# Kernel optimization log

Hardware: AMD Instinct MI355X
Metric: run time of the kernel (lower is better)

## Reference

```python
import jax, jax.numpy as jnp
import numpy as np

N = 100000      # num_nodes
E = 400000      # num edges
HID = 128       # hidden_channels (== in_channels, memory dim)
OUT = 64        # out_channels (per head)
HEADS = 4
HD = HEADS * OUT  # 256, TransformerConv concat output dim


def _lin(k, fan_in, fan_out):
    return jax.random.normal(k, (fan_in, fan_out), jnp.float32) * 0.02


def setup_inputs() -> dict:
    key = jax.random.key(0)
    ks = jax.random.split(key, 16)
    return {
        "edge_index": jax.random.randint(ks[0], (2, E), 0, N, dtype=jnp.int64),
        "edge_time": jax.random.randint(ks[1], (E, 1), 0, 1000000, dtype=jnp.int64),
        "x": jax.random.normal(ks[2], (N, HID), jnp.float32),
        "memory": jax.random.normal(ks[3], (N, HID), jnp.float32),  # TGN memory table (detached in fwd)
        # TransformerConv params (lin_query / lin_key / lin_value / lin_skip, all with bias)
        "Wq": _lin(ks[4], HID, HD), "bq": jnp.zeros((HD,), jnp.float32),
        "Wk": _lin(ks[5], HID, HD), "bk": jnp.zeros((HD,), jnp.float32),
        "Wv": _lin(ks[6], HID, HD), "bv": jnp.zeros((HD,), jnp.float32),
        "Wskip": _lin(ks[7], HID, HD), "bskip": jnp.zeros((HD,), jnp.float32),
        # rating MLP: Linear(512,128) -> ReLU -> Linear(128,64) -> ReLU -> Linear(64,1)
        "W1": _lin(ks[8], 2 * HD, 128), "b1": jnp.zeros((128,), jnp.float32),
        "W2": _lin(ks[9], 128, 64), "b2": jnp.zeros((64,), jnp.float32),
        "W3": _lin(ks[10], 64, 1), "b3": jnp.zeros((1,), jnp.float32),
    }


def reference(edge_index, edge_time, x, memory,
              Wq, bq, Wk, bk, Wv, bv, Wskip, bskip,
              W1, b1, W2, b2, W3, b3):
    src, dst = edge_index[0], edge_index[1]
    n = x.shape[0]

    # x = memory.detach() + x
    h = memory + x  # [N, HID]

    # TransformerConv (heads=4, concat=True, root_weight=True)
    q = (h @ Wq + bq).reshape(n, HEADS, OUT)
    k = (h @ Wk + bk).reshape(n, HEADS, OUT)
    v = (h @ Wv + bv).reshape(n, HEADS, OUT)

    # per-edge attention scores: messages flow src -> dst, softmax over in-edges of dst
    scores = jnp.sum(q[dst] * k[src], axis=-1) / jnp.sqrt(jnp.float32(OUT))  # [E, H]
    smax = jax.ops.segment_max(scores, dst, num_segments=n)                   # [N, H]
    e = jnp.exp(scores - smax[dst])
    denom = jax.ops.segment_sum(e, dst, num_segments=n)
    alpha = e / (denom[dst] + 1e-16)                                          # [E, H]

    agg = jax.ops.segment_sum(alpha[:, :, None] * v[src], dst, num_segments=n)  # [N, H, OUT]
    out = agg.reshape(n, HD) + (h @ Wskip + bskip)                              # skip connection

    # interaction embeddings + MLP head (dropout inactive at eval)
    inter = jnp.concatenate([out[src], out[dst]], axis=-1)  # [E, 512]
    hdd = jax.nn.relu(inter @ W1 + b1)
    hdd = jax.nn.relu(hdd @ W2 + b2)
    rating = jax.nn.sigmoid(hdd @ W3 + b3) * 4.0 + 1.0
    return rating[:, 0]
```

## Files before the change

kernel.cpp:

```cpp
#include <hip/hip_runtime.h>
#include <math.h>

#define N_NODES 100000
#define N_EDGES 400000
#define HID 128
#define HEADS 4
#define OUT_C 64
#define HD 256
#define SCAN_CHUNK 1024
#define NB_SCAN ((N_NODES + SCAN_CHUNK - 1) / SCAN_CHUNK)

typedef __attribute__((ext_vector_type(8))) short bf16x8;
typedef __attribute__((ext_vector_type(4))) float f32x4;

__device__ __forceinline__ unsigned short fbf(float f) {
    unsigned u = __float_as_uint(f);
    unsigned r = (u + 0x7fffu + ((u >> 16) & 1u)) >> 16;
    return (unsigned short)r;
}
__device__ __forceinline__ float bf2f(unsigned short u) {
    return __uint_as_float(((unsigned)u) << 16);
}

__device__ __forceinline__ void gl_lds16(const void* g, void* l) {
    __builtin_amdgcn_global_load_lds(
        (const __attribute__((address_space(1))) unsigned int*)g,
        (__attribute__((address_space(3))) unsigned int*)l,
        16, 0, 0);
}

__global__ __launch_bounds__(256) void init_zero(int* __restrict__ deg,
                                                 int* __restrict__ cursor) {
    int i = blockIdx.x * 256 + threadIdx.x;
    if (i < N_NODES) { deg[i] = 0; cursor[i] = 0; }
}

__global__ __launch_bounds__(256) void k_deg(const int* __restrict__ ei,
                                             int* __restrict__ deg) {
    int e = blockIdx.x * 256 + threadIdx.x;
    if (e < N_EDGES) atomicAdd(&deg[ei[N_EDGES + e]], 1);
}

__global__ __launch_bounds__(256) void k_scan1(const int* __restrict__ deg,
                                               int* __restrict__ rp,
                                               int* __restrict__ bsum) {
    __shared__ int ts[256];
    int b = blockIdx.x, t = threadIdx.x;
    int base = b * SCAN_CHUNK + t * 4;
    int vv[4];
    int s = 0;
#pragma unroll
    for (int i = 0; i < 4; ++i) {
        int d = (base + i < N_NODES) ? deg[base + i] : 0;
        vv[i] = s;
        s += d;
    }
    ts[t] = s;
    __syncthreads();
    for (int off = 1; off < 256; off <<= 1) {
        int x = (t >= off) ? ts[t - off] : 0;
        __syncthreads();
        ts[t] += x;
        __syncthreads();
    }
    int ex = ts[t] - s;
#pragma unroll
    for (int i = 0; i < 4; ++i)
        if (base + i < N_NODES) rp[base + i] = ex + vv[i];
    if (t == 255) bsum[b] = ts[255];
}

__global__ __launch_bounds__(256) void k_scan2(int* __restrict__ bsum) {
    __shared__ int ts[256];
    int t = threadIdx.x;
    int v = (t < NB_SCAN) ? bsum[t] : 0;
    ts[t] = v;
    __syncthreads();
    for (int off = 1; off < 256; off <<= 1) {
        int x = (t >= off) ? ts[t - off] : 0;
        __syncthreads();
        ts[t] += x;
        __syncthreads();
    }
    if (t < NB_SCAN) bsum[t] = ts[t] - v;
}

__global__ __launch_bounds__(256) void k_scan3(int* __restrict__ rp,
                                               const int* __restrict__ bsum) {
    int i = blockIdx.x * 256 + threadIdx.x;
    if (i < N_NODES) rp[i] += bsum[i / SCAN_CHUNK];
}

__global__ __launch_bounds__(256) void k_bucket(const int* __restrict__ ei,
                                                const int* __restrict__ rp,
                                                int* __restrict__ cursor,
                                                int* __restrict__ csr_src,
                                                int* __restrict__ csr_dst,
                                                int* __restrict__ csr_eid) {
    int e = blockIdx.x * 256 + threadIdx.x;
    if (e >= N_EDGES) return;
    int src = ei[e];
    int d   = ei[N_EDGES + e];
    int idx = atomicAdd(&cursor[d], 1);
    int s   = rp[d] + idx;
    csr_src[s] = src;
    csr_dst[s] = d;
    csr_eid[s] = e;
}

__global__ __launch_bounds__(256) void pack_wg(
    const float* __restrict__ Wq, const float* __restrict__ Wk,
    const float* __restrict__ Wv, const float* __restrict__ Ws,
    unsigned short* __restrict__ Wp) {
    int i = blockIdx.x * 256 + threadIdx.x;
    if (i >= 16384) return;
    int lane = i & 63, nt = (i >> 6) & 15, kt = (i >> 10) & 3, z = i >> 12;
    const float* W = (z == 0) ? Wq : (z == 1) ? Wk : (z == 2) ? Wv : Ws;
    int q = lane >> 4, c = lane & 15;
#pragma unroll
    for (int j = 0; j < 8; ++j)
        Wp[i * 8 + j] = fbf(W[(kt * 32 + q * 8 + j) * HD + nt * 16 + c]);
}

__global__ __launch_bounds__(256) void pack_wc(const float* __restrict__ W1,
                                               unsigned short* __restrict__ Wcp) {
    int i = blockIdx.x * 256 + threadIdx.x;
    if (i >= 8192) return;
    int lane = i & 63, nt = (i >> 6) & 15, kt = i >> 10;
    int q = lane >> 4, c = lane & 15;
    int n = nt * 16 + c;
#pragma unroll
    for (int j = 0; j < 8; ++j) {
        int k = kt * 32 + q * 8 + j;
        float v = (n < 128) ? W1[k * 128 + n] : W1[(k + 256) * 128 + (n - 128)];
        Wcp[i * 8 + j] = fbf(v);
    }
}

__global__ __launch_bounds__(256) void pack_w2(const float* __restrict__ W2,
                                               unsigned short* __restrict__ W2p) {
    int i = blockIdx.x * 256 + threadIdx.x;
    if (i >= 1024) return;
    int lane = i & 63, nt = (i >> 6) & 3, kt = i >> 8;
    int q = lane >> 4, c = lane & 15;
#pragma unroll
    for (int j = 0; j < 8; ++j)
        W2p[i * 8 + j] = fbf(W2[(kt * 32 + q * 8 + j) * 64 + nt * 16 + c]);
}

__global__ __launch_bounds__(256) void k_pre(const float* __restrict__ x,
                                             const float* __restrict__ mem,
                                             unsigned short* __restrict__ H) {
    int idx = blockIdx.x * 256 + threadIdx.x;
    if (idx >= N_NODES * HID / 8) return;
    const float4* x4 = (const float4*)x;
    const float4* m4 = (const float4*)mem;
    float4 a0 = x4[(size_t)idx * 2],     a1 = x4[(size_t)idx * 2 + 1];
    float4 b0 = m4[(size_t)idx * 2],     b1 = m4[(size_t)idx * 2 + 1];
    bf16x8 hv;
    hv[0] = (short)fbf(a0.x + b0.x); hv[1] = (short)fbf(a0.y + b0.y);
    hv[2] = (short)fbf(a0.z + b0.z); hv[3] = (short)fbf(a0.w + b0.w);
    hv[4] = (short)fbf(a1.x + b1.x); hv[5] = (short)fbf(a1.y + b1.y);
    hv[6] = (short)fbf(a1.z + b1.z); hv[7] = (short)fbf(a1.w + b1.w);
    *(bf16x8*)&H[(size_t)idx * 8] = hv;
}

__global__ __launch_bounds__(256, 4) void gemm4(
    const unsigned short* __restrict__ H,
    const unsigned short* __restrict__ Wp,
    const float* __restrict__ bq, const float* __restrict__ bk,
    const float* __restrict__ bv, const float* __restrict__ bs,
    unsigned short* __restrict__ Q, unsigned short* __restrict__ KV,
    unsigned short* __restrict__ S)
{
    __shared__ __align__(16) short sh[4 * 64 * 68];
    short* As = sh;

    const int t = threadIdx.x;
    const int w = t >> 6, l = t & 63;
    const int q = l >> 4, c = l & 15;
    const int z  = blockIdx.y;
    const int m0 = blockIdx.x * 64;

#pragma unroll
    for (int i = 0; i < 4; ++i) {
        int rbase = w * 16 + i * 4;
        int r  = rbase + (l >> 4);
        int gr = m0 + r; if (gr >= N_NODES) gr = N_NODES - 1;
        int ks = (l & 15) ^ (r & 7);
        gl_lds16(&H[(size_t)gr * HID + ks * 8], &As[rbase * 128]);
    }

    unsigned short* Oz; int rs, coff; const float* bz;
    if      (z == 0) { Oz = Q;  rs = 256; coff = 0;   bz = bq; }
    else if (z == 1) { Oz = KV; rs = 512; coff = 0;   bz = bk; }
    else if (z == 2) { Oz = KV; rs = 512; coff = 256; bz = bv; }
    else             { Oz = S;  rs = 256; coff = 0;   bz = bs; }
    float bb[4];
#pragma unroll
    for (int nt = 0; nt < 4; ++nt) bb[nt] = bz[w * 64 + nt * 16 + c];

    f32x4 acc[4][4];
#pragma unroll
    for (int mt = 0; mt < 4; ++mt)
#pragma unroll
        for (int nt = 0; nt < 4; ++nt) acc[mt][nt] = (f32x4){0.f, 0.f, 0.f, 0.f};

    __syncthreads();

#pragma unroll
    for (int kt = 0; kt < 4; ++kt) {
        bf16x8 af[4];
#pragma unroll
        for (int mt = 0; mt < 4; ++mt) {
            int row  = mt * 16 + c;
            int slot = (kt * 4 + q) ^ (row & 7);
            af[mt] = *(const bf16x8*)&As[row * 128 + slot * 8];
        }
#pragma unroll
        for (int nt = 0; nt < 4; ++nt) {
            bf16x8 bw8 = *(const bf16x8*)&Wp[(size_t)(((z * 4 + kt) * 16 + w * 4 + nt) * 64 + l) * 8];
#pragma unroll
            for (int mt = 0; mt < 4; ++mt)
                acc[mt][nt] = __builtin_amdgcn_mfma_f32_16x16x32_bf16(af[mt], bw8, acc[mt][nt], 0, 0, 0);
        }
    }
    __syncthreads();

    short* slab = &sh[w * 64 * 68];
#pragma unroll
    for (int nt = 0; nt < 4; ++nt)
#pragma unroll
        for (int mt = 0; mt < 4; ++mt)
#pragma unroll
            for (int r = 0; r < 4; ++r)
                slab[(mt * 16 + q * 4 + r) * 68 + nt * 16 + c] =
                    (short)fbf(acc[mt][nt][r] + bb[nt]);

    const int srow = l >> 3, schk = l & 7;
#pragma unroll
    for (int j = 0; j < 8; ++j) {
        int row = j * 8 + srow;
        int gr  = m0 + row;
        if (gr < N_NODES)
            *(bf16x8*)&Oz[(size_t)gr * rs + coff + w * 64 + schk * 8] =
                *(const bf16x8*)&slab[row * 68 + schk * 8];
    }
}

__global__ __launch_bounds__(256) void k_attn(
    const int* __restrict__ rp, const int* __restrict__ deg,
    const int* __restrict__ csr_src,
    const unsigned short* __restrict__ Q, const unsigned short* __restrict__ KV,
    const unsigned short* __restrict__ S,
    unsigned short* __restrict__ out)
{
    int node = blockIdx.x * 4 + (threadIdx.x >> 6);
    int l = threadIdx.x & 63;
    if (node >= N_NODES) return;
    int start = rp[node];
    int cnt   = deg[node];

    float q0, q1, q2, q3;
    {
        ushort4 u = *(const ushort4*)&Q[(size_t)node * HD + l * 4];
        q0 = bf2f(u.x); q1 = bf2f(u.y); q2 = bf2f(u.z); q3 = bf2f(u.w);
    }

    float d = 0.f;
    float a0 = 0.f, a1 = 0.f, a2 = 0.f, a3 = 0.f;

    int i = 0;
    for (; i + 2 <= cnt; i += 2) {
        int s0 = csr_src[start + i];
        int s1 = csr_src[start + i + 1];
        const unsigned short* kv0 = &KV[(size_t)s0 * 512 + l * 4];
        const unsigned short* kv1 = &KV[(size_t)s1 * 512 + l * 4];
        ushort4 ku0 = *(const ushort4*)kv0;
        ushort4 vu0 = *(const ushort4*)(kv0 + 256);
        ushort4 ku1 = *(const ushort4*)kv1;
        ushort4 vu1 = *(const ushort4*)(kv1 + 256);
        float sA = q0 * bf2f(ku0.x) + q1 * bf2f(ku0.y) + q2 * bf2f(ku0.z) + q3 * bf2f(ku0.w);
        float sB = q0 * bf2f(ku1.x) + q1 * bf2f(ku1.y) + q2 * bf2f(ku1.z) + q3 * bf2f(ku1.w);
        sA += __shfl_xor(sA, 1);  sB += __shfl_xor(sB, 1);
        sA += __shfl_xor(sA, 2);  sB += __shfl_xor(sB, 2);
        sA += __shfl_xor(sA, 4);  sB += __shfl_xor(sB, 4);
        sA += __shfl_xor(sA, 8);  sB += __shfl_xor(sB, 8);
        float eA = __expf(sA * 0.125f);
        float eB = __expf(sB * 0.125f);
        d += eA + eB;
        a0 += eA * bf2f(vu0.x) + eB * bf2f(vu1.x);
        a1 += eA * bf2f(vu0.y) + eB * bf2f(vu1.y);
        a2 += eA * bf2f(vu0.z) + eB * bf2f(vu1.z);
        a3 += eA * bf2f(vu0.w) + eB * bf2f(vu1.w);
    }
    if (i < cnt) {
        int s0 = csr_src[start + i];
        const unsigned short* kv0 = &KV[(size_t)s0 * 512 + l * 4];
        ushort4 ku0 = *(const ushort4*)kv0;
        ushort4 vu0 = *(const ushort4*)(kv0 + 256);
        float sA = q0 * bf2f(ku0.x) + q1 * bf2f(ku0.y) + q2 * bf2f(ku0.z) + q3 * bf2f(ku0.w);
        sA += __shfl_xor(sA, 1);
        sA += __shfl_xor(sA, 2);
        sA += __shfl_xor(sA, 4);
        sA += __shfl_xor(sA, 8);
        float eA = __expf(sA * 0.125f);
        d += eA;
        a0 += eA * bf2f(vu0.x);
        a1 += eA * bf2f(vu0.y);
        a2 += eA * bf2f(vu0.z);
        a3 += eA * bf2f(vu0.w);
    }

    float inv = 1.f / (d + 1e-16f);
    ushort4 su = *(const ushort4*)&S[(size_t)node * HD + l * 4];
    ushort4 ov = make_ushort4(fbf(bf2f(su.x) + a0 * inv),
                              fbf(bf2f(su.y) + a1 * inv),
                              fbf(bf2f(su.z) + a2 * inv),
                              fbf(bf2f(su.w) + a3 * inv));
    *(ushort4*)&out[(size_t)node * HD + l * 4] = ov;
}

__global__ __launch_bounds__(256, 4) void pd_gemm(
    const unsigned short* __restrict__ outb,
    const unsigned short* __restrict__ Wcp,
    unsigned short* __restrict__ PD)
{
    __shared__ __align__(16) short sh[4 * 64 * 68];
    short* As = sh;

    const int t = threadIdx.x;
    const int w = t >> 6, l = t & 63;
    const int q = l >> 4, c = l & 15;
    const int m0 = blockIdx.x * 64;

#pragma unroll
    for (int i = 0; i < 8; ++i) {
        int rbase = w * 16 + i * 2;
        int r  = rbase + (l >> 5);
        int gr = m0 + r; if (gr >= N_NODES) gr = N_NODES - 1;
        int s  = (l & 31) ^ (r & 7);
        gl_lds16(&outb[(size_t)gr * HD + s * 8], &As[rbase * 256]);
    }

    f32x4 acc[4][4];
#pragma unroll
    for (int mt = 0; mt < 4; ++mt)
#pragma unroll
        for (int nt = 0; nt < 4; ++nt) acc[mt][nt] = (f32x4){0.f, 0.f, 0.f, 0.f};

    __syncthreads();

#pragma unroll
    for (int kt = 0; kt < 8; ++kt) {
        bf16x8 af[4];
#pragma unroll
        for (int mt = 0; mt < 4; ++mt) {
            int row  = mt * 16 + c;
            int slot = (kt * 4 + q) ^ (row & 7);
            af[mt] = *(const bf16x8*)&As[row * 256 + slot * 8];
        }
#pragma unroll
        for (int nt = 0; nt < 4; ++nt) {
            int ntg = w * 4 + nt;
            bf16x8 bv8 = *(const bf16x8*)&Wcp[(size_t)((kt * 16 + ntg) * 64 + l) * 8];
#pragma unroll
            for (int mt = 0; mt < 4; ++mt)
                acc[mt][nt] = __builtin_amdgcn_mfma_f32_16x16x32_bf16(af[mt], bv8, acc[mt][nt], 0, 0, 0);
        }
    }
    __syncthreads();

    short* slab = &sh[w * 64 * 68];
#pragma unroll
    for (int nt = 0; nt < 4; ++nt)
#pragma unroll
        for (int mt = 0; mt < 4; ++mt)
#pragma unroll
            for (int r = 0; r < 4; ++r)
                slab[(mt * 16 + q * 4 + r) * 68 + nt * 16 + c] =
                    (short)fbf(acc[mt][nt][r]);
    const int srow = l >> 3, schk = l & 7;
#pragma unroll
    for (int j = 0; j < 8; ++j) {
        int row = j * 8 + srow;
        int gr = m0 + row;
        if (gr < N_NODES)
            *(bf16x8*)&PD[(size_t)gr * HD + w * 64 + schk * 8] =
                *(const bf16x8*)&slab[row * 68 + schk * 8];
    }
}

__global__ __launch_bounds__(256) void edge_mlp_pd(
    const int* __restrict__ csr_src, const int* __restrict__ csr_dst,
    const int* __restrict__ csr_eid,
    const unsigned short* __restrict__ PD,
    const float* __restrict__ b1,
    const unsigned short* __restrict__ W2p, const float* __restrict__ b2,
    const float* __restrict__ W3, const float* __restrict__ b3,
    float* __restrict__ rating)
{
    __shared__ __align__(16) char lds[64 * 136 * 2];
    short* h1t = (short*)lds;
    float* h2s = (float*)lds;

    const int t = threadIdx.x;
    const int w = t >> 6, l = t & 63;
    const int q = l >> 4, c = l & 15;
    const int e0 = blockIdx.x * 64;

#pragma unroll
    for (int j = 0; j < 4; ++j) {
        int idx = t + j * 256;
        int row = idx >> 4, ch = idx & 15;
        int src = csr_src[e0 + row];
        int dst = csr_dst[e0 + row];
        bf16x8 pv = *(const bf16x8*)&PD[(size_t)src * HD + ch * 8];
        bf16x8 dv = *(const bf16x8*)&PD[(size_t)dst * HD + 128 + ch * 8];
        float4 ba = *(const float4*)&b1[ch * 8];
        float4 bb = *(const float4*)&b1[ch * 8 + 4];
        bf16x8 hv;
        hv[0] = (short)fbf(fmaxf(bf2f((unsigned short)pv[0]) + bf2f((unsigned short)dv[0]) + ba.x, 0.f));
        hv[1] = (short)fbf(fmaxf(bf2f((unsigned short)pv[1]) + bf2f((unsigned short)dv[1]) + ba.y, 0.f));
        hv[2] = (short)fbf(fmaxf(bf2f((unsigned short)pv[2]) + bf2f((unsigned short)dv[2]) + ba.z, 0.f));
        hv[3] = (short)fbf(fmaxf(bf2f((unsigned short)pv[3]) + bf2f((unsigned short)dv[3]) + ba.w, 0.f));
        hv[4] = (short)fbf(fmaxf(bf2f((unsigned short)pv[4]) + bf2f((unsigned short)dv[4]) + bb.x, 0.f));
        hv[5] = (short)fbf(fmaxf(bf2f((unsigned short)pv[5]) + bf2f((unsigned short)dv[5]) + bb.y, 0.f));
        hv[6] = (short)fbf(fmaxf(bf2f((unsigned short)pv[6]) + bf2f((unsigned short)dv[6]) + bb.z, 0.f));
        hv[7] = (short)fbf(fmaxf(bf2f((unsigned short)pv[7]) + bf2f((unsigned short)dv[7]) + bb.w, 0.f));
        *(bf16x8*)&h1t[row * 136 + ch * 8] = hv;
    }
    __syncthreads();

    f32x4 acc2[4];
#pragma unroll
    for (int i = 0; i < 4; ++i) acc2[i] = (f32x4){0.f, 0.f, 0.f, 0.f};
#pragma unroll
    for (int kt = 0; kt < 4; ++kt) {
        bf16x8 av = *(const bf16x8*)&h1t[(w * 16 + c) * 136 + kt * 32 + q * 8];
#pragma unroll
        for (int nt = 0; nt < 4; ++nt) {
            bf16x8 bv = *(const bf16x8*)&W2p[(size_t)((kt * 4 + nt) * 64 + l) * 8];
            acc2[nt] = __builtin_amdgcn_mfma_f32_16x16x32_bf16(av, bv, acc2[nt], 0, 0, 0);
        }
    }
    __syncthreads();

#pragma unroll
    for (int nt = 0; nt < 4; ++nt) {
        float bv = b2[nt * 16 + c];
#pragma unroll
        for (int r = 0; r < 4; ++r)
            h2s[(w * 16 + q * 4 + r) * 65 + nt * 16 + c] = fmaxf(acc2[nt][r] + bv, 0.f);
    }
    __syncthreads();

    if (t < 64) {
        float a = b3[0];
#pragma unroll 8
        for (int kk = 0; kk < 64; ++kk)
            a += h2s[t * 65 + kk] * W3[kk];
        rating[csr_eid[e0 + t]] = 4.f / (1.f + __expf(-a)) + 1.f;
    }
}

extern "C" void kernel_launch(void* const* d_in, const int* in_sizes, int n_in,
                              void* d_out, int out_size, void* d_ws, size_t ws_size,
                              hipStream_t stream) {
    const int*   ei  = (const int*)d_in[0];
    const float* x   = (const float*)d_in[2];
    const float* mem = (const float*)d_in[3];
    const float* Wq  = (const float*)d_in[4];
    const float* bq  = (const float*)d_in[5];
    const float* Wk  = (const float*)d_in[6];
    const float* bk  = (const float*)d_in[7];
    const float* Wv  = (const float*)d_in[8];
    const float* bv  = (const float*)d_in[9];
    const float* Ws  = (const float*)d_in[10];
    const float* bs  = (const float*)d_in[11];
    const float* W1  = (const float*)d_in[12];
    const float* b1  = (const float*)d_in[13];
    const float* W2  = (const float*)d_in[14];
    const float* b2  = (const float*)d_in[15];
    const float* W3  = (const float*)d_in[16];
    const float* b3  = (const float*)d_in[17];
    float* rating = (float*)d_out;

    unsigned short* Q = (unsigned short*)d_ws;
    const size_t NHDe = (size_t)N_NODES * HD;
    unsigned short* KV = Q + NHDe;
    unsigned short* S  = KV + 2 * NHDe;
    unsigned short* H  = S + NHDe;
    int* rp      = (int*)(H + (size_t)N_NODES * HID);
    int* deg     = rp + N_NODES;
    int* cursor  = deg + N_NODES;
    int* csr_src = cursor + N_NODES;
    int* csr_dst = csr_src + N_EDGES;
    int* csr_eid = csr_dst + N_EDGES;
    int* bsum    = csr_eid + N_EDGES;
    unsigned short* Wp  = (unsigned short*)(bsum + 128);
    unsigned short* Wcp = Wp + 16384 * 8;
    unsigned short* W2p = Wcp + 8192 * 8;
    unsigned short* PD  = KV;

    const int nblk  = (N_NODES + 255) / 256;
    const int eblk  = (N_EDGES + 255) / 256;
    const int wgrid = (N_NODES + 3) / 4;
    const int pblk  = (N_NODES * HID / 8 + 255) / 256;

    init_zero<<<nblk, 256, 0, stream>>>(deg, cursor);
    k_deg<<<eblk, 256, 0, stream>>>(ei, deg);
    k_scan1<<<NB_SCAN, 256, 0, stream>>>(deg, rp, bsum);
    k_scan2<<<1, 256, 0, stream>>>(bsum);
    k_scan3<<<nblk, 256, 0, stream>>>(rp, bsum);
    k_bucket<<<eblk, 256, 0, stream>>>(ei, rp, cursor, csr_src, csr_dst, csr_eid);
    pack_wg<<<64, 256, 0, stream>>>(Wq, Wk, Wv, Ws, Wp);
    pack_wc<<<32, 256, 0, stream>>>(W1, Wcp);
    pack_w2<<<4, 256, 0, stream>>>(W2, W2p);

    k_pre<<<pblk, 256, 0, stream>>>(x, mem, H);

    gemm4<<<dim3((N_NODES + 63) / 64, 4), dim3(256), 0, stream>>>(
        H, Wp, bq, bk, bv, bs, Q, KV, S);

    k_attn<<<wgrid, 256, 0, stream>>>(rp, deg, csr_src, Q, KV, S, Q);

    pd_gemm<<<(N_NODES + 63) / 64, 256, 0, stream>>>(Q, Wcp, PD);

    edge_mlp_pd<<<N_EDGES / 64, 256, 0, stream>>>(
        csr_src, csr_dst, csr_eid, PD, b1, W2p, b2, W3, b3, rating);
}
```

Baseline: 410.1 us.

## Interleave K and V per lane, fold scan fixup and weight packing kernels

The GEMM epilogue now writes K and V interleaved per 4-element chunk, so each attention lane fetches its K and V values with a single 16-byte load, and the attention loop is unrolled to four edges with the 1/sqrt(d) scale folded into q. The scan fixup kernel is removed by adding the block offset at use sites in bucket and attention. The three weight-packing kernels are merged into one launch. This trades launch count and gather transactions for slightly more index arithmetic and 8-byte split stores in the GEMM epilogue.

```diff
diff --git a/kernel.cpp b/kernel.cpp
--- a/kernel.cpp
+++ b/kernel.cpp
@@ -85,14 +85,9 @@
     if (t < NB_SCAN) bsum[t] = ts[t] - v;
 }
 
-__global__ __launch_bounds__(256) void k_scan3(int* __restrict__ rp,
-                                               const int* __restrict__ bsum) {
-    int i = blockIdx.x * 256 + threadIdx.x;
-    if (i < N_NODES) rp[i] += bsum[i / SCAN_CHUNK];
-}
-
 __global__ __launch_bounds__(256) void k_bucket(const int* __restrict__ ei,
                                                 const int* __restrict__ rp,
+                                                const int* __restrict__ bsum,
                                                 int* __restrict__ cursor,
                                                 int* __restrict__ csr_src,
                                                 int* __restrict__ csr_dst,
@@ -102,50 +97,44 @@
     int src = ei[e];
     int d   = ei[N_EDGES + e];
     int idx = atomicAdd(&cursor[d], 1);
-    int s   = rp[d] + idx;
+    int s   = rp[d] + bsum[d >> 10] + idx;
     csr_src[s] = src;
     csr_dst[s] = d;
     csr_eid[s] = e;
 }
 
-__global__ __launch_bounds__(256) void pack_wg(
+__global__ __launch_bounds__(256) void pack_all(
     const float* __restrict__ Wq, const float* __restrict__ Wk,
     const float* __restrict__ Wv, const float* __restrict__ Ws,
-    unsigned short* __restrict__ Wp) {
+    const float* __restrict__ W1, const float* __restrict__ W2,
+    unsigned short* __restrict__ Wp, unsigned short* __restrict__ Wcp,
+    unsigned short* __restrict__ W2p) {
     int i = blockIdx.x * 256 + threadIdx.x;
-    if (i >= 16384) return;
-    int lane = i & 63, nt = (i >> 6) & 15, kt = (i >> 10) & 3, z = i >> 12;
-    const float* W = (z == 0) ? Wq : (z == 1) ? Wk : (z == 2) ? Wv : Ws;
+    int lane = i & 63;
     int q = lane >> 4, c = lane & 15;
-#pragma unroll
-    for (int j = 0; j < 8; ++j)
-        Wp[i * 8 + j] = fbf(W[(kt * 32 + q * 8 + j) * HD + nt * 16 + c]);
-}
-
-__global__ __launch_bounds__(256) void pack_wc(const float* __restrict__ W1,
-                                               unsigned short* __restrict__ Wcp) {
-    int i = blockIdx.x * 256 + threadIdx.x;
-    if (i >= 8192) return;
-    int lane = i & 63, nt = (i >> 6) & 15, kt = i >> 10;
-    int q = lane >> 4, c = lane & 15;
-    int n = nt * 16 + c;
-#pragma unroll
-    for (int j = 0; j < 8; ++j) {
-        int k = kt * 32 + q * 8 + j;
-        float v = (n < 128) ? W1[k * 128 + n] : W1[(k + 256) * 128 + (n - 128)];
-        Wcp[i * 8 + j] = fbf(v);
-    }
-}
-
-__global__ __launch_bounds__(256) void pack_w2(const float* __restrict__ W2,
-                                               unsigned short* __restrict__ W2p) {
-    int i = blockIdx.x * 256 + threadIdx.x;
-    if (i >= 1024) return;
-    int lane = i & 63, nt = (i >> 6) & 3, kt = i >> 8;
-    int q = lane >> 4, c = lane & 15;
-#pragma unroll
-    for (int j = 0; j < 8; ++j)
-        W2p[i * 8 + j] = fbf(W2[(kt * 32 + q * 8 + j) * 64 + nt * 16 + c]);
+    if (i < 16384) {
+        int nt = (i >> 6) & 15, kt = (i >> 10) & 3, z = i >> 12;
+        const float* W = (z == 0) ? Wq : (z == 1) ? Wk : (z == 2) ? Wv : Ws;
+#pragma unroll
+        for (int j = 0; j < 8; ++j)
+            Wp[i * 8 + j] = fbf(W[(kt * 32 + q * 8 + j) * HD + nt * 16 + c]);
+    } else if (i < 24576) {
+        int ii = i - 16384;
+        int nt = (ii >> 6) & 15, kt = ii >> 10;
+        int n = nt * 16 + c;
+#pragma unroll
+        for (int j = 0; j < 8; ++j) {
+            int k = kt * 32 + q * 8 + j;
+            float v = (n < 128) ? W1[k * 128 + n] : W1[(k + 256) * 128 + (n - 128)];
+            Wcp[ii * 8 + j] = fbf(v);
+        }
+    } else if (i < 25600) {
+        int ii = i - 24576;
+        int nt = (ii >> 6) & 3, kt = ii >> 8;
+#pragma unroll
+        for (int j = 0; j < 8; ++j)
+            W2p[ii * 8 + j] = fbf(W2[(kt * 32 + q * 8 + j) * 64 + nt * 16 + c]);
+    }
 }
 
 __global__ __launch_bounds__(256) void k_pre(const float* __restrict__ x,
@@ -191,11 +180,7 @@
         gl_lds16(&H[(size_t)gr * HID + ks * 8], &As[rbase * 128]);
     }
 
-    unsigned short* Oz; int rs, coff; const float* bz;
-    if      (z == 0) { Oz = Q;  rs = 256; coff = 0;   bz = bq; }
-    else if (z == 1) { Oz = KV; rs = 512; coff = 0;   bz = bk; }
-    else if (z == 2) { Oz = KV; rs = 512; coff = 256; bz = bv; }
-    else             { Oz = S;  rs = 256; coff = 0;   bz = bs; }
+    const float* bz = (z == 0) ? bq : (z == 1) ? bk : (z == 2) ? bv : bs;
     float bb[4];
 #pragma unroll
     for (int nt = 0; nt < 4; ++nt) bb[nt] = bz[w * 64 + nt * 16 + c];
@@ -238,19 +223,35 @@
                     (short)fbf(acc[mt][nt][r] + bb[nt]);
 
     const int srow = l >> 3, schk = l & 7;
-#pragma unroll
-    for (int j = 0; j < 8; ++j) {
-        int row = j * 8 + srow;
-        int gr  = m0 + row;
-        if (gr < N_NODES)
-            *(bf16x8*)&Oz[(size_t)gr * rs + coff + w * 64 + schk * 8] =
-                *(const bf16x8*)&slab[row * 68 + schk * 8];
+    if (z == 1 || z == 2) {
+        const int voff = (z == 2) ? 4 : 0;
+#pragma unroll
+        for (int j = 0; j < 8; ++j) {
+            int row = j * 8 + srow;
+            int gr  = m0 + row;
+            if (gr < N_NODES) {
+                const short* sp = &slab[row * 68 + schk * 8];
+                size_t base = (size_t)gr * 512 + w * 128 + schk * 16 + voff;
+                *(ushort4*)&KV[base]     = *(const ushort4*)sp;
+                *(ushort4*)&KV[base + 8] = *(const ushort4*)(sp + 4);
+            }
+        }
+    } else {
+        unsigned short* Oz = (z == 0) ? Q : S;
+#pragma unroll
+        for (int j = 0; j < 8; ++j) {
+            int row = j * 8 + srow;
+            int gr  = m0 + row;
+            if (gr < N_NODES)
+                *(bf16x8*)&Oz[(size_t)gr * HD + w * 64 + schk * 8] =
+                    *(const bf16x8*)&slab[row * 68 + schk * 8];
+        }
     }
 }
 
 __global__ __launch_bounds__(256) void k_attn(
-    const int* __restrict__ rp, const int* __restrict__ deg,
-    const int* __restrict__ csr_src,
+    const int* __restrict__ rp, const int* __restrict__ bsum,
+    const int* __restrict__ deg, const int* __restrict__ csr_src,
     const unsigned short* __restrict__ Q, const unsigned short* __restrict__ KV,
     const unsigned short* __restrict__ S,
     unsigned short* __restrict__ out)
@@ -258,58 +259,71 @@
     int node = blockIdx.x * 4 + (threadIdx.x >> 6);
     int l = threadIdx.x & 63;
     if (node >= N_NODES) return;
-    int start = rp[node];
+    int start = rp[node] + bsum[node >> 10];
     int cnt   = deg[node];
 
     float q0, q1, q2, q3;
     {
         ushort4 u = *(const ushort4*)&Q[(size_t)node * HD + l * 4];
-        q0 = bf2f(u.x); q1 = bf2f(u.y); q2 = bf2f(u.z); q3 = bf2f(u.w);
+        q0 = bf2f(u.x) * 0.125f; q1 = bf2f(u.y) * 0.125f;
+        q2 = bf2f(u.z) * 0.125f; q3 = bf2f(u.w) * 0.125f;
     }
 
     float d = 0.f;
     float a0 = 0.f, a1 = 0.f, a2 = 0.f, a3 = 0.f;
 
     int i = 0;
-    for (; i + 2 <= cnt; i += 2) {
+    for (; i + 4 <= cnt; i += 4) {
         int s0 = csr_src[start + i];
         int s1 = csr_src[start + i + 1];
-        const unsigned short* kv0 = &KV[(size_t)s0 * 512 + l * 4];
-        const unsigned short* kv1 = &KV[(size_t)s1 * 512 + l * 4];
-        ushort4 ku0 = *(const ushort4*)kv0;
-        ushort4 vu0 = *(const ushort4*)(kv0 + 256);
-        ushort4 ku1 = *(const ushort4*)kv1;
-        ushort4 vu1 = *(const ushort4*)(kv1 + 256);
-        float sA = q0 * bf2f(ku0.x) + q1 * bf2f(ku0.y) + q2 * bf2f(ku0.z) + q3 * bf2f(ku0.w);
-        float sB = q0 * bf2f(ku1.x) + q1 * bf2f(ku1.y) + q2 * bf2f(ku1.z) + q3 * bf2f(ku1.w);
-        sA += __shfl_xor(sA, 1);  sB += __shfl_xor(sB, 1);
-        sA += __shfl_xor(sA, 2);  sB += __shfl_xor(sB, 2);
-        sA += __shfl_xor(sA, 4);  sB += __shfl_xor(sB, 4);
-        sA += __shfl_xor(sA, 8);  sB += __shfl_xor(sB, 8);
-        float eA = __expf(sA * 0.125f);
-        float eB = __expf(sB * 0.125f);
-        d += eA + eB;
-        a0 += eA * bf2f(vu0.x) + eB * bf2f(vu1.x);
-        a1 += eA * bf2f(vu0.y) + eB * bf2f(vu1.y);
-        a2 += eA * bf2f(vu0.z) + eB * bf2f(vu1.z);
-        a3 += eA * bf2f(vu0.w) + eB * bf2f(vu1.w);
-    }
-    if (i < cnt) {
+        int s2 = csr_src[start + i + 2];
+        int s3 = csr_src[start + i + 3];
+        bf16x8 k0 = *(const bf16x8*)&KV[(size_t)s0 * 512 + l * 8];
+        bf16x8 k1 = *(const bf16x8*)&KV[(size_t)s1 * 512 + l * 8];
+        bf16x8 k2 = *(const bf16x8*)&KV[(size_t)s2 * 512 + l * 8];
+        bf16x8 k3 = *(const bf16x8*)&KV[(size_t)s3 * 512 + l * 8];
+        float sA = q0 * bf2f((unsigned short)k0[0]) + q1 * bf2f((unsigned short)k0[1])
+                 + q2 * bf2f((unsigned short)k0[2]) + q3 * bf2f((unsigned short)k0[3]);
+        float sB = q0 * bf2f((unsigned short)k1[0]) + q1 * bf2f((unsigned short)k1[1])
+                 + q2 * bf2f((unsigned short)k1[2]) + q3 * bf2f((unsigned short)k1[3]);
+        float sC = q0 * bf2f((unsigned short)k2[0]) + q1 * bf2f((unsigned short)k2[1])
+                 + q2 * bf2f((unsigned short)k2[2]) + q3 * bf2f((unsigned short)k2[3]);
+        float sD = q0 * bf2f((unsigned short)k3[0]) + q1 * bf2f((unsigned short)k3[1])
+                 + q2 * bf2f((unsigned short)k3[2]) + q3 * bf2f((unsigned short)k3[3]);
+        sA += __shfl_xor(sA, 1); sB += __shfl_xor(sB, 1);
+        sC += __shfl_xor(sC, 1); sD += __shfl_xor(sD, 1);
+        sA += __shfl_xor(sA, 2); sB += __shfl_xor(sB, 2);
+        sC += __shfl_xor(sC, 2); sD += __shfl_xor(sD, 2);
+        sA += __shfl_xor(sA, 4); sB += __shfl_xor(sB, 4);
+        sC += __shfl_xor(sC, 4); sD += __shfl_xor(sD, 4);
+        sA += __shfl_xor(sA, 8); sB += __shfl_xor(sB, 8);
+        sC += __shfl_xor(sC, 8); sD += __shfl_xor(sD, 8);
+        float eA = __expf(sA), eB = __expf(sB), eC = __expf(sC), eD = __expf(sD);
+        d += (eA + eB) + (eC + eD);
+        a0 += eA * bf2f((unsigned short)k0[4]) + eB * bf2f((unsigned short)k1[4])
+            + eC * bf2f((unsigned short)k2[4]) + eD * bf2f((unsigned short)k3[4]);
+        a1 += eA * bf2f((unsigned short)k0[5]) + eB * bf2f((unsigned short)k1[5])
+            + eC * bf2f((unsigned short)k2[5]) + eD * bf2f((unsigned short)k3[5]);
+        a2 += eA * bf2f((unsigned short)k0[6]) + eB * bf2f((unsigned short)k1[6])
+            + eC * bf2f((unsigned short)k2[6]) + eD * bf2f((unsigned short)k3[6]);
+        a3 += eA * bf2f((unsigned short)k0[7]) + eB * bf2f((unsigned short)k1[7])
+            + eC * bf2f((unsigned short)k2[7]) + eD * bf2f((unsigned short)k3[7]);
+    }
+    for (; i < cnt; ++i) {
         int s0 = csr_src[start + i];
-        const unsigned short* kv0 = &KV[(size_t)s0 * 512 + l * 4];
-        ushort4 ku0 = *(const ushort4*)kv0;
-        ushort4 vu0 = *(const ushort4*)(kv0 + 256);
-        float sA = q0 * bf2f(ku0.x) + q1 * bf2f(ku0.y) + q2 * bf2f(ku0.z) + q3 * bf2f(ku0.w);
+        bf16x8 k0 = *(const bf16x8*)&KV[(size_t)s0 * 512 + l * 8];
+        float sA = q0 * bf2f((unsigned short)k0[0]) + q1 * bf2f((unsigned short)k0[1])
+                 + q2 * bf2f((unsigned short)k0[2]) + q3 * bf2f((unsigned short)k0[3]);
         sA += __shfl_xor(sA, 1);
         sA += __shfl_xor(sA, 2);
         sA += __shfl_xor(sA, 4);
         sA += __shfl_xor(sA, 8);
-        float eA = __expf(sA * 0.125f);
+        float eA = __expf(sA);
         d += eA;
-        a0 += eA * bf2f(vu0.x);
-        a1 += eA * bf2f(vu0.y);
-        a2 += eA * bf2f(vu0.z);
-        a3 += eA * bf2f(vu0.w);
+        a0 += eA * bf2f((unsigned short)k0[4]);
+        a1 += eA * bf2f((unsigned short)k0[5]);
+        a2 += eA * bf2f((unsigned short)k0[6]);
+        a3 += eA * bf2f((unsigned short)k0[7]);
     }
 
     float inv = 1.f / (d + 1e-16f);
@@ -512,18 +526,15 @@
     k_deg<<<eblk, 256, 0, stream>>>(ei, deg);
     k_scan1<<<NB_SCAN, 256, 0, stream>>>(deg, rp, bsum);
     k_scan2<<<1, 256, 0, stream>>>(bsum);
-    k_scan3<<<nblk, 256, 0, stream>>>(rp, bsum);
-    k_bucket<<<eblk, 256, 0, stream>>>(ei, rp, cursor, csr_src, csr_dst, csr_eid);
-    pack_wg<<<64, 256, 0, stream>>>(Wq, Wk, Wv, Ws, Wp);
-    pack_wc<<<32, 256, 0, stream>>>(W1, Wcp);
-    pack_w2<<<4, 256, 0, stream>>>(W2, W2p);
+    k_bucket<<<eblk, 256, 0, stream>>>(ei, rp, bsum, cursor, csr_src, csr_dst, csr_eid);
+    pack_all<<<100, 256, 0, stream>>>(Wq, Wk, Wv, Ws, W1, W2, Wp, Wcp, W2p);
 
     k_pre<<<pblk, 256, 0, stream>>>(x, mem, H);
 
     gemm4<<<dim3((N_NODES + 63) / 64, 4), dim3(256), 0, stream>>>(
         H, Wp, bq, bk, bv, bs, Q, KV, S);
 
-    k_attn<<<wgrid, 256, 0, stream>>>(rp, deg, csr_src, Q, KV, S, Q);
+    k_attn<<<wgrid, 256, 0, stream>>>(rp, bsum, deg, csr_src, Q, KV, S, Q);
 
     pd_gemm<<<(N_NODES + 63) / 64, 256, 0, stream>>>(Q, Wcp, PD);
 
```

New measurement: 456.3 us. 1.11x slower.
